# Kernel optimization log

Hardware: AMD Instinct MI355X
Metric: run time of the kernel (lower is better)

## Reference

```python
import jax, jax.numpy as jnp
import numpy as np
from jax import lax

K = 3          # kernel size
PAD = 1        # 'same' padding for k=3: (1,1,1,1)
STRIDE = 1
DIL = 1
OFFSET_SIZE = 2 * K * K  # deformable_groups=1


def setup_inputs() -> dict:
    key = jax.random.key(0)
    k1, k2, k3, k4 = jax.random.split(key, 4)
    B, H, W, C = 8, 64, 64, 256
    F = 256
    inputs = jax.random.normal(k1, (B, H, W, C), dtype=jnp.float32)
    # offset/mask branch conv: small weights so sampled offsets are modest
    om_kernel = jax.random.normal(k2, (K, K, C, OFFSET_SIZE * 3 // 2), dtype=jnp.float32) * 0.01
    om_bias = jnp.zeros((OFFSET_SIZE * 3 // 2,), dtype=jnp.float32)
    stdv = 1.0 / np.sqrt(K * K * C)
    kernel = jax.random.uniform(k3, (K * K * C, F), dtype=jnp.float32, minval=-stdv, maxval=stdv)
    bias = jax.random.normal(k4, (1, 1, 1, F), dtype=jnp.float32) * 0.01
    return {"inputs": inputs, "om_kernel": om_kernel, "om_bias": om_bias,
            "kernel": kernel, "bias": bias}


def _dcnv2(x, om_kernel, om_bias, kernel, bias):
    B, H, W, C = x.shape
    # offset/mask branch (same conv geometry as the deformable conv)
    om = lax.conv_general_dilated(
        x, om_kernel, window_strides=(STRIDE, STRIDE),
        padding=((PAD, PAD), (PAD, PAD)), rhs_dilation=(DIL, DIL),
        dimension_numbers=('NHWC', 'HWIO', 'NHWC')) + om_bias
    OH, OW = om.shape[1], om.shape[2]
    KK = K * K
    offset = om[..., :OFFSET_SIZE].reshape(B, OH, OW, KK, 2)  # (dy, dx) per kernel point
    mask = jax.nn.sigmoid(om[..., OFFSET_SIZE:]) * 2.0         # [B,OH,OW,KK]

    # base sampling grid per output pixel and kernel point
    kk = jnp.arange(KK)
    ky = (kk // K).astype(jnp.float32)
    kx = (kk % K).astype(jnp.float32)
    base_y = jnp.arange(OH, dtype=jnp.float32)[:, None] * STRIDE - PAD + ky[None, :] * DIL  # [OH,KK]
    base_x = jnp.arange(OW, dtype=jnp.float32)[:, None] * STRIDE - PAD + kx[None, :] * DIL  # [OW,KK]

    py = base_y[None, :, None, :] + offset[..., 0]  # [B,OH,OW,KK]
    px = base_x[None, None, :, :] + offset[..., 1]

    y0 = jnp.floor(py); x0 = jnp.floor(px)
    wy1 = py - y0; wy0 = 1.0 - wy1
    wx1 = px - x0; wx0 = 1.0 - wx1

    bi = jnp.arange(B)[:, None, None, None]

    def gather(yi, xi):
        # zero-padded bilinear corner fetch
        valid = (yi >= 0) & (yi <= H - 1) & (xi >= 0) & (xi <= W - 1)
        yc = jnp.clip(yi, 0, H - 1).astype(jnp.int32)
        xc = jnp.clip(xi, 0, W - 1).astype(jnp.int32)
        v = x[bi, yc, xc]  # [B,OH,OW,KK,C]
        return v * valid[..., None].astype(x.dtype)

    y1 = y0 + 1.0; x1 = x0 + 1.0
    cols = (gather(y0, x0) * (wy0 * wx0)[..., None]
            + gather(y0, x1) * (wy0 * wx1)[..., None]
            + gather(y1, x0) * (wy1 * wx0)[..., None]
            + gather(y1, x1) * (wy1 * wx1)[..., None])
    cols = cols * mask[..., None]  # modulation, [B,OH,OW,KK,C]

    out = cols.reshape(B, OH, OW, KK * C) @ kernel  # [B,OH,OW,F]
    return out + bias


def reference(inputs, om_kernel, om_bias, kernel, bias):
    return _dcnv2(inputs, om_kernel, om_bias, kernel, bias)
```

## Files before the change

kernel.cpp:

```cpp
#include <hip/hip_runtime.h>
#include <math.h>


#define BB 8
#define HH 64
#define WW 64
#define CIN 256
#define FF 256
#define KPTS 9
#define OCH 27
#define MT 64
#define NS2 36

typedef _Float16 half8  __attribute__((ext_vector_type(8)));
typedef _Float16 half4v __attribute__((ext_vector_type(4)));
typedef float    floatx4 __attribute__((ext_vector_type(4)));

__device__ __forceinline__ int aoff(int m, int g) {
    return m * 64 + ((g ^ (m & 7)) << 3);
}

__device__ __forceinline__ half8 splat8(_Float16 v) {
    half8 r = {v, v, v, v, v, v, v, v};
    return r;
}

#define XBLK 4096
__global__ __launch_bounds__(256) void convert_all(
    const float* __restrict__ x, const float* __restrict__ wmat,
    const float* __restrict__ omw,
    _Float16* __restrict__ xh, _Float16* __restrict__ wsB, _Float16* __restrict__ wsOM)
{
    const int bid = blockIdx.x;
    if (bid < XBLK) {
        if (xh == nullptr) return;
        const size_t i = ((size_t)bid * 256 + threadIdx.x) * 8;
        const floatx4 a = *(const floatx4*)(x + i);
        const floatx4 b = *(const floatx4*)(x + i + 4);
        half8 h;
        h[0] = (_Float16)a.x; h[1] = (_Float16)a.y; h[2] = (_Float16)a.z; h[3] = (_Float16)a.w;
        h[4] = (_Float16)b.x; h[5] = (_Float16)b.y; h[6] = (_Float16)b.z; h[7] = (_Float16)b.w;
        *(half8*)(xh + i) = h;
    } else if (bid < XBLK + 288) {
        const int kg = bid - XBLK;
        const int n  = threadIdx.x;
        half8 h;
        #pragma unroll
        for (int j = 0; j < 8; ++j)
            h[j] = (_Float16)wmat[(size_t)(kg * 8 + j) * FF + n];
        ((half8*)wsB)[(size_t)kg * FF + n] = h;
    } else {
        const int t = (bid - XBLK - 288) * 256 + threadIdx.x;
        const int k = t >> 5, n = t & 31;
        const float v = (n < OCH) ? omw[k * OCH + n] : 0.f;
        wsOM[((size_t)(k >> 3) * 32 + n) * 8 + (k & 7)] = (_Float16)v;
    }
}

template <bool F16X>
__global__ __launch_bounds__(512, 4) void dcn_mfma3(
    const float* __restrict__ x,
    const _Float16* __restrict__ xh,
    const float* __restrict__ omb,
    const _Float16* __restrict__ wsB,
    const _Float16* __restrict__ wsOM,
    const float* __restrict__ bias,
    float* __restrict__ out)
{
    __shared__ _Float16 Ah0[MT * 64];
    __shared__ _Float16 Ah1[MT * 64];
    __shared__ float    om_s[MT][28];
    __shared__ half4v   cwS[MT][KPTS];
    __shared__ int4     caS[MT][KPTS];

    const int tid  = threadIdx.x;
    const int w    = tid >> 6;
    const int lane = tid & 63;
    const int q    = lane >> 4;
    const int lr   = lane & 15;
    const int ms   = tid >> 3;
    const int qc   = tid & 7;

    const int p  = blockIdx.x;
    const int b  = p & 7;
    const int oh = p >> 3;
    const int pbase = (b * HH + oh) * WW;

    const half8* wsOM8 = (const half8*)wsOM;
    const half8* wsB8  = (const half8*)wsB;

    const int mt1 = w & 3;
    const int nt1 = w >> 2;
    floatx4 acc1 = {0.f, 0.f, 0.f, 0.f};

    auto load1 = [&](int sp) -> half8 {
        sp = sp < NS2 - 1 ? sp : NS2 - 1;
        const int kk = sp >> 2, cb = (sp & 3) << 6;
        const int ky = kk / 3, kx = kk - ky * 3;
        const int iy = oh - 1 + ky, ix = ms - 1 + kx;
        half8 v = {(_Float16)0, (_Float16)0, (_Float16)0, (_Float16)0,
                   (_Float16)0, (_Float16)0, (_Float16)0, (_Float16)0};
        if (iy >= 0 && iy < HH && ix >= 0 && ix < WW) {
            const int idx = ((b * HH + iy) * WW + ix) * CIN + cb + qc * 8;
            if constexpr (F16X) {
                v = *(const half8*)(xh + idx);
            } else {
                const floatx4 lo = *(const floatx4*)(x + idx);
                const floatx4 hi = *(const floatx4*)(x + idx + 4);
                v[0] = (_Float16)lo.x; v[1] = (_Float16)lo.y;
                v[2] = (_Float16)lo.z; v[3] = (_Float16)lo.w;
                v[4] = (_Float16)hi.x; v[5] = (_Float16)hi.y;
                v[6] = (_Float16)hi.z; v[7] = (_Float16)hi.w;
            }
        }
        return v;
    };
    auto loadB1 = [&](int sp, half8& b0, half8& b1) {
        sp = sp < NS2 - 1 ? sp : NS2 - 1;
        b0 = wsOM8[(sp * 8 + q) * 32 + nt1 * 16 + lr];
        b1 = wsOM8[(sp * 8 + 4 + q) * 32 + nt1 * 16 + lr];
    };

    half8 vp;
    half8 bo00, bo01, bo10, bo11;
    {
        const half8 v0 = load1(0);
        *(half8*)(Ah0 + aoff(ms, qc)) = v0;
        vp = load1(1);
        loadB1(0, bo00, bo01);
    }
    for (int s = 0; s < NS2; s += 2) {
        __syncthreads();
        *(half8*)(Ah1 + aoff(ms, qc)) = vp;
        vp = load1(s + 2);
        loadB1(s + 1, bo10, bo11);
        {
            const half8 a0 = *(const half8*)(Ah0 + aoff(mt1 * 16 + lr, q));
            const half8 a1 = *(const half8*)(Ah0 + aoff(mt1 * 16 + lr, 4 + q));
            acc1 = __builtin_amdgcn_mfma_f32_16x16x32_f16(a0, bo00, acc1, 0, 0, 0);
            acc1 = __builtin_amdgcn_mfma_f32_16x16x32_f16(a1, bo01, acc1, 0, 0, 0);
        }
        __syncthreads();
        *(half8*)(Ah0 + aoff(ms, qc)) = vp;
        vp = load1(s + 3);
        loadB1(s + 2, bo00, bo01);
        {
            const half8 a0 = *(const half8*)(Ah1 + aoff(mt1 * 16 + lr, q));
            const half8 a1 = *(const half8*)(Ah1 + aoff(mt1 * 16 + lr, 4 + q));
            acc1 = __builtin_amdgcn_mfma_f32_16x16x32_f16(a0, bo10, acc1, 0, 0, 0);
            acc1 = __builtin_amdgcn_mfma_f32_16x16x32_f16(a1, bo11, acc1, 0, 0, 0);
        }
    }
    {
        const int och = nt1 * 16 + lr;
        if (och < OCH) {
            const float ob = omb[och];
            #pragma unroll
            for (int reg = 0; reg < 4; ++reg) {
                const int m = mt1 * 16 + q * 4 + reg;
                om_s[m][och] = acc1[reg] + ob;
            }
        }
    }
    __syncthreads();

    for (int i = tid; i < MT * KPTS; i += 512) {
        const int m = i / KPTS, kk = i % KPTS;
        const int ky = kk / 3, kx = kk - ky * 3;
        const float dy = om_s[m][2 * kk];
        const float dx = om_s[m][2 * kk + 1];
        const float mask = 2.f / (1.f + __expf(-om_s[m][18 + kk]));
        const float py = (float)(oh - 1 + ky) + dy;
        const float px = (float)(m - 1 + kx) + dx;
        const float y0f = floorf(py), x0f = floorf(px);
        const float wy1 = py - y0f, wx1 = px - x0f;
        const float wy0 = 1.f - wy1, wx0 = 1.f - wx1;
        const int y0 = (int)y0f, x0 = (int)x0f;
        const int y1 = y0 + 1, x1 = x0 + 1;
        const bool vy0 = (y0 >= 0) && (y0 < HH);
        const bool vy1 = (y1 >= 0) && (y1 < HH);
        const bool vx0 = (x0 >= 0) && (x0 < WW);
        const bool vx1 = (x1 >= 0) && (x1 < WW);
        const int y0c = min(max(y0, 0), HH - 1), y1c = min(max(y1, 0), HH - 1);
        const int x0c = min(max(x0, 0), WW - 1), x1c = min(max(x1, 0), WW - 1);
        const int rb = b * HH;
        int4 ca;
        ca.x = ((rb + y0c) * WW + x0c) * CIN;
        ca.y = ((rb + y0c) * WW + x1c) * CIN;
        ca.z = ((rb + y1c) * WW + x0c) * CIN;
        ca.w = ((rb + y1c) * WW + x1c) * CIN;
        half4v cw;
        cw.x = (_Float16)((vy0 && vx0) ? mask * wy0 * wx0 : 0.f);
        cw.y = (_Float16)((vy0 && vx1) ? mask * wy0 * wx1 : 0.f);
        cw.z = (_Float16)((vy1 && vx0) ? mask * wy1 * wx0 : 0.f);
        cw.w = (_Float16)((vy1 && vx1) ? mask * wy1 * wx1 : 0.f);
        caS[m][kk] = ca;
        cwS[m][kk] = cw;
    }
    __syncthreads();

    floatx4 acc[4][2];
    #pragma unroll
    for (int mt = 0; mt < 4; ++mt)
        #pragma unroll
        for (int nt = 0; nt < 2; ++nt)
            acc[mt][nt] = (floatx4){0.f, 0.f, 0.f, 0.f};

    const int n0w = w * 32;

    half8   pc0, pc1, pc2, pc3;
    floatx4 fa0, fb0, fa1, fb1, fa2, fb2, fa3, fb3;
    half4v  pcw;

    auto pre2 = [&](int sp) {
        sp = sp < NS2 - 1 ? sp : NS2 - 1;
        const int kk = sp >> 2;
        const int co = ((sp & 3) << 6) + qc * 8;
        const int4 ca = caS[ms][kk];
        pcw = cwS[ms][kk];
        if constexpr (F16X) {
            pc0 = *(const half8*)(xh + ca.x + co);
            pc1 = *(const half8*)(xh + ca.y + co);
            pc2 = *(const half8*)(xh + ca.z + co);
            pc3 = *(const half8*)(xh + ca.w + co);
        } else {
            fa0 = *(const floatx4*)(x + ca.x + co); fb0 = *(const floatx4*)(x + ca.x + co + 4);
            fa1 = *(const floatx4*)(x + ca.y + co); fb1 = *(const floatx4*)(x + ca.y + co + 4);
            fa2 = *(const floatx4*)(x + ca.z + co); fb2 = *(const floatx4*)(x + ca.z + co + 4);
            fa3 = *(const floatx4*)(x + ca.w + co); fb3 = *(const floatx4*)(x + ca.w + co + 4);
        }
    };
    auto comb = [&]() -> half8 {
        if constexpr (F16X) {
            const half8 w0 = splat8(pcw.x), w1 = splat8(pcw.y);
            const half8 w2 = splat8(pcw.z), w3 = splat8(pcw.w);
            return pc0 * w0 + pc1 * w1 + pc2 * w2 + pc3 * w3;
        } else {
            const float w0 = (float)pcw.x, w1 = (float)pcw.y;
            const float w2 = (float)pcw.z, w3 = (float)pcw.w;
            const floatx4 lo = w0 * fa0 + w1 * fa1 + w2 * fa2 + w3 * fa3;
            const floatx4 hi = w0 * fb0 + w1 * fb1 + w2 * fb2 + w3 * fb3;
            half8 r;
            r[0] = (_Float16)lo.x; r[1] = (_Float16)lo.y;
            r[2] = (_Float16)lo.z; r[3] = (_Float16)lo.w;
            r[4] = (_Float16)hi.x; r[5] = (_Float16)hi.y;
            r[6] = (_Float16)hi.z; r[7] = (_Float16)hi.w;
            return r;
        }
    };

    half8 bPa[2][2], bPb[2][2];
    auto loadB2 = [&](int sp, half8 (&bP)[2][2]) {
        sp = sp < NS2 - 1 ? sp : NS2 - 1;
        #pragma unroll
        for (int kh = 0; kh < 2; ++kh)
            #pragma unroll
            for (int nt = 0; nt < 2; ++nt)
                bP[kh][nt] = wsB8[(size_t)(sp * 8 + kh * 4 + q) * FF + n0w + nt * 16 + lr];
    };

    {
        pre2(0);
        const half8 v0 = comb();
        *(half8*)(Ah0 + aoff(ms, qc)) = v0;
        pre2(1);
        loadB2(0, bPa);
    }
    for (int s = 0; s < NS2; s += 2) {
        __syncthreads();
        {
            const half8 v = comb();
            *(half8*)(Ah1 + aoff(ms, qc)) = v;
        }
        pre2(s + 2);
        loadB2(s + 1, bPb);
        #pragma unroll
        for (int kh = 0; kh < 2; ++kh) {
            half8 afr[4];
            #pragma unroll
            for (int mt = 0; mt < 4; ++mt)
                afr[mt] = *(const half8*)(Ah0 + aoff(mt * 16 + lr, kh * 4 + q));
            #pragma unroll
            for (int nt = 0; nt < 2; ++nt)
                #pragma unroll
                for (int mt = 0; mt < 4; ++mt)
                    acc[mt][nt] = __builtin_amdgcn_mfma_f32_16x16x32_f16(afr[mt], bPa[kh][nt], acc[mt][nt], 0, 0, 0);
        }
        __syncthreads();
        {
            const half8 v = comb();
            *(half8*)(Ah0 + aoff(ms, qc)) = v;
        }
        pre2(s + 3);
        loadB2(s + 2, bPa);
        #pragma unroll
        for (int kh = 0; kh < 2; ++kh) {
            half8 afr[4];
            #pragma unroll
            for (int mt = 0; mt < 4; ++mt)
                afr[mt] = *(const half8*)(Ah1 + aoff(mt * 16 + lr, kh * 4 + q));
            #pragma unroll
            for (int nt = 0; nt < 2; ++nt)
                #pragma unroll
                for (int mt = 0; mt < 4; ++mt)
                    acc[mt][nt] = __builtin_amdgcn_mfma_f32_16x16x32_f16(afr[mt], bPb[kh][nt], acc[mt][nt], 0, 0, 0);
        }
    }

    #pragma unroll
    for (int nt = 0; nt < 2; ++nt) {
        const int f = n0w + nt * 16 + lr;
        const float bv = bias[f];
        #pragma unroll
        for (int mt = 0; mt < 4; ++mt)
            #pragma unroll
            for (int reg = 0; reg < 4; ++reg) {
                const int m = mt * 16 + q * 4 + reg;
                out[(size_t)(pbase + m) * FF + f] = acc[mt][nt][reg] + bv;
            }
    }
}

#define MTILE 32
#define CHUNK 64
#define NCHUNK (CIN / CHUNK)

__global__ __launch_bounds__(256) void dcn_fused(
    const float* __restrict__ x, const float* __restrict__ omw,
    const float* __restrict__ omb, const float* __restrict__ wmat,
    const float* __restrict__ bias, float* __restrict__ out)
{
    __shared__ float A[CHUNK][MTILE + 1];
    __shared__ float om_s[MTILE][28];
    __shared__ float cw[MTILE][4];
    __shared__ int   ca[MTILE][4];

    const int tid = threadIdx.x;
    const int pbase = blockIdx.x * MTILE;
    const int ccid = tid & 63;
    const int mg2 = tid >> 6;
    const int och = tid & 31;
    const int mg1 = tid >> 5;
    float acc1[4] = {0.f, 0.f, 0.f, 0.f};

    for (int kk = 0; kk < KPTS; ++kk) {
        const int ky = kk / 3, kx = kk % 3;
        for (int ch = 0; ch < NCHUNK; ++ch) {
            const int cbase = ch * CHUNK;
            __syncthreads();
            #pragma unroll
            for (int i = 0; i < 8; ++i) {
                const int m = mg2 * 8 + i;
                const int pp = pbase + m;
                const int bb = pp >> 12, oh = (pp >> 6) & 63, ow = pp & 63;
                const int iy = oh - 1 + ky, ix = ow - 1 + kx;
                float v = 0.f;
                if (iy >= 0 && iy < HH && ix >= 0 && ix < WW)
                    v = x[((bb * HH + iy) * WW + ix) * CIN + cbase + ccid];
                A[ccid][m] = v;
            }
            __syncthreads();
            if (och < OCH) {
                for (int cc = 0; cc < CHUNK; ++cc) {
                    const float bv = omw[((kk * CIN) + cbase + cc) * OCH + och];
                    #pragma unroll
                    for (int i = 0; i < 4; ++i)
                        acc1[i] += A[cc][mg1 * 4 + i] * bv;
                }
            }
        }
    }
    __syncthreads();
    if (och < OCH) {
        const float ob = omb[och];
        #pragma unroll
        for (int i = 0; i < 4; ++i)
            om_s[mg1 * 4 + i][och] = acc1[i] + ob;
    }
    __syncthreads();

    const int f4 = (tid & 63) * 4;
    const int mgc = tid >> 6;
    float acc[8][4];
    #pragma unroll
    for (int j = 0; j < 8; ++j)
        #pragma unroll
        for (int i = 0; i < 4; ++i) acc[j][i] = 0.f;

    for (int kk = 0; kk < KPTS; ++kk) {
        if (tid < MTILE) {
            const int m = tid;
            const int pp = pbase + m;
            const int bb = pp >> 12, oh = (pp >> 6) & 63, ow = pp & 63;
            const int ky = kk / 3, kx = kk % 3;
            const float dy = om_s[m][2 * kk];
            const float dx = om_s[m][2 * kk + 1];
            const float mask = 2.f / (1.f + __expf(-om_s[m][18 + kk]));
            const float py = (float)(oh - 1 + ky) + dy;
            const float px = (float)(ow - 1 + kx) + dx;
            const float y0f = floorf(py), x0f = floorf(px);
            const float wy1 = py - y0f, wx1 = px - x0f;
            const float wy0 = 1.f - wy1, wx0 = 1.f - wx1;
            const int y0 = (int)y0f, x0 = (int)x0f;
            const int y1 = y0 + 1, x1 = x0 + 1;
            const bool vy0 = (y0 >= 0) && (y0 < HH);
            const bool vy1 = (y1 >= 0) && (y1 < HH);
            const bool vx0 = (x0 >= 0) && (x0 < WW);
            const bool vx1 = (x1 >= 0) && (x1 < WW);
            const int y0c = min(max(y0, 0), HH - 1), y1c = min(max(y1, 0), HH - 1);
            const int x0c = min(max(x0, 0), WW - 1), x1c = min(max(x1, 0), WW - 1);
            const int rb = bb * HH;
            ca[m][0] = ((rb + y0c) * WW + x0c) * CIN;
            ca[m][1] = ((rb + y0c) * WW + x1c) * CIN;
            ca[m][2] = ((rb + y1c) * WW + x0c) * CIN;
            ca[m][3] = ((rb + y1c) * WW + x1c) * CIN;
            cw[m][0] = (vy0 && vx0) ? mask * wy0 * wx0 : 0.f;
            cw[m][1] = (vy0 && vx1) ? mask * wy0 * wx1 : 0.f;
            cw[m][2] = (vy1 && vx0) ? mask * wy1 * wx0 : 0.f;
            cw[m][3] = (vy1 && vx1) ? mask * wy1 * wx1 : 0.f;
        }
        for (int ch = 0; ch < NCHUNK; ++ch) {
            const int cbase = ch * CHUNK;
            __syncthreads();
            #pragma unroll
            for (int i = 0; i < 8; ++i) {
                const int m = mg2 * 8 + i;
                const int cidx = cbase + ccid;
                const float v = cw[m][0] * x[ca[m][0] + cidx]
                              + cw[m][1] * x[ca[m][1] + cidx]
                              + cw[m][2] * x[ca[m][2] + cidx]
                              + cw[m][3] * x[ca[m][3] + cidx];
                A[ccid][m] = v;
            }
            __syncthreads();
            const float* brow = wmat + (size_t)(kk * CIN + cbase) * FF + f4;
            for (int cc = 0; cc < CHUNK; ++cc) {
                const float4 bv = *(const float4*)(brow + cc * FF);
                #pragma unroll
                for (int j = 0; j < 8; ++j) {
                    const float a = A[cc][mgc * 8 + j];
                    acc[j][0] += a * bv.x;
                    acc[j][1] += a * bv.y;
                    acc[j][2] += a * bv.z;
                    acc[j][3] += a * bv.w;
                }
            }
        }
    }

    const float4 bb4 = *(const float4*)(bias + f4);
    #pragma unroll
    for (int j = 0; j < 8; ++j) {
        const int m = mgc * 8 + j;
        const int pp = pbase + m;
        float4 o;
        o.x = acc[j][0] + bb4.x;
        o.y = acc[j][1] + bb4.y;
        o.z = acc[j][2] + bb4.z;
        o.w = acc[j][3] + bb4.w;
        *(float4*)(out + (size_t)pp * FF + f4) = o;
    }
}

extern "C" void kernel_launch(void* const* d_in, const int* in_sizes, int n_in,
                              void* d_out, int out_size, void* d_ws, size_t ws_size,
                              hipStream_t stream) {
    const float* x    = (const float*)d_in[0];
    const float* omw  = (const float*)d_in[1];
    const float* omb  = (const float*)d_in[2];
    const float* wmat = (const float*)d_in[3];
    const float* bias = (const float*)d_in[4];
    float* out = (float*)d_out;

    const size_t needB  = (size_t)2304 * FF * sizeof(_Float16);
    const size_t needOM = (size_t)288 * 32 * 8 * sizeof(_Float16);
    const size_t needX  = (size_t)BB * HH * WW * CIN * sizeof(_Float16);

    if (ws_size >= needB + needOM + needX) {
        _Float16* wsB  = (_Float16*)d_ws;
        _Float16* wsOM = (_Float16*)((char*)d_ws + needB);
        _Float16* xh   = (_Float16*)((char*)d_ws + needB + needOM);
        convert_all<<<XBLK + 288 + 288, 256, 0, stream>>>(x, wmat, omw, xh, wsB, wsOM);
        dcn_mfma3<true><<<BB * HH, 512, 0, stream>>>(x, xh, omb, wsB, wsOM, bias, out);
    } else if (ws_size >= needB + needOM) {
        _Float16* wsB  = (_Float16*)d_ws;
        _Float16* wsOM = (_Float16*)((char*)d_ws + needB);
        convert_all<<<XBLK + 288 + 288, 256, 0, stream>>>(x, wmat, omw, nullptr, wsB, wsOM);
        dcn_mfma3<false><<<BB * HH, 512, 0, stream>>>(x, nullptr, omb, wsB, wsOM, bias, out);
    } else {
        const int nblocks = (BB * HH * WW) / MTILE;
        dcn_fused<<<nblocks, 256, 0, stream>>>(x, omw, omb, wmat, bias, out);
    }
}
```

Baseline: 163.1 us.

## Retile MFMA warps to 2x4 M/N split and reorder K steps channel-major

Each of the 8 warps now covers 32 rows by 64 output channels instead of 64 rows by 32 channels. This halves the per-warp LDS A-fragment reads and doubles B-fragment register loads. The K-step order changes from kernel-point-major to channel-chunk-major via a divide-by-9 trick, so consecutive steps visit different sampling points. B fragments are now loaded just before use instead of prefetched one step ahead, which may expose global load latency.

```diff
diff --git a/kernel.cpp b/kernel.cpp
--- a/kernel.cpp
+++ b/kernel.cpp
@@ -58,7 +58,7 @@
 }
 
 template <bool F16X>
-__global__ __launch_bounds__(512, 4) void dcn_mfma3(
+__global__ __launch_bounds__(512, 4) void dcn_mfma4(
     const float* __restrict__ x,
     const _Float16* __restrict__ xh,
     const float* __restrict__ omb,
@@ -199,14 +199,16 @@
     }
     __syncthreads();
 
-    floatx4 acc[4][2];
+    floatx4 acc[2][4];
     #pragma unroll
-    for (int mt = 0; mt < 4; ++mt)
-        #pragma unroll
-        for (int nt = 0; nt < 2; ++nt)
-            acc[mt][nt] = (floatx4){0.f, 0.f, 0.f, 0.f};
-
-    const int n0w = w * 32;
+    for (int t = 0; t < 2; ++t)
+        #pragma unroll
+        for (int nt = 0; nt < 4; ++nt)
+            acc[t][nt] = (floatx4){0.f, 0.f, 0.f, 0.f};
+
+    const int mh  = w & 1;
+    const int nh  = w >> 1;
+    const int n0w = nh * 64;
 
     half8   pc0, pc1, pc2, pc3;
     floatx4 fa0, fb0, fa1, fb1, fa2, fb2, fa3, fb3;
@@ -214,8 +216,9 @@
 
     auto pre2 = [&](int sp) {
         sp = sp < NS2 - 1 ? sp : NS2 - 1;
-        const int kk = sp >> 2;
-        const int co = ((sp & 3) << 6) + qc * 8;
+        const int c  = (sp * 456) >> 12;
+        const int kk = sp - c * 9;
+        const int co = c * 64 + qc * 8;
         const int4 ca = caS[ms][kk];
         pcw = cwS[ms][kk];
         if constexpr (F16X) {
@@ -249,14 +252,16 @@
         }
     };
 
-    half8 bPa[2][2], bPb[2][2];
-    auto loadB2 = [&](int sp, half8 (&bP)[2][2]) {
-        sp = sp < NS2 - 1 ? sp : NS2 - 1;
+    half8 bP[2][4];
+    auto loadB2 = [&](int sp) {
+        const int c  = (sp * 456) >> 12;
+        const int kk = sp - c * 9;
+        const int r8 = kk * 32 + c * 8;
         #pragma unroll
         for (int kh = 0; kh < 2; ++kh)
             #pragma unroll
-            for (int nt = 0; nt < 2; ++nt)
-                bP[kh][nt] = wsB8[(size_t)(sp * 8 + kh * 4 + q) * FF + n0w + nt * 16 + lr];
+            for (int nt = 0; nt < 4; ++nt)
+                bP[kh][nt] = wsB8[(size_t)(r8 + kh * 4 + q) * FF + n0w + nt * 16 + lr];
     };
 
     {
@@ -264,7 +269,6 @@
         const half8 v0 = comb();
         *(half8*)(Ah0 + aoff(ms, qc)) = v0;
         pre2(1);
-        loadB2(0, bPa);
     }
     for (int s = 0; s < NS2; s += 2) {
         __syncthreads();
@@ -272,51 +276,51 @@
             const half8 v = comb();
             *(half8*)(Ah1 + aoff(ms, qc)) = v;
         }
+        loadB2(s);
         pre2(s + 2);
-        loadB2(s + 1, bPb);
         #pragma unroll
         for (int kh = 0; kh < 2; ++kh) {
-            half8 afr[4];
-            #pragma unroll
-            for (int mt = 0; mt < 4; ++mt)
-                afr[mt] = *(const half8*)(Ah0 + aoff(mt * 16 + lr, kh * 4 + q));
-            #pragma unroll
-            for (int nt = 0; nt < 2; ++nt)
+            half8 afr[2];
+            #pragma unroll
+            for (int t = 0; t < 2; ++t)
+                afr[t] = *(const half8*)(Ah0 + aoff((mh * 2 + t) * 16 + lr, kh * 4 + q));
+            #pragma unroll
+            for (int nt = 0; nt < 4; ++nt)
                 #pragma unroll
-                for (int mt = 0; mt < 4; ++mt)
-                    acc[mt][nt] = __builtin_amdgcn_mfma_f32_16x16x32_f16(afr[mt], bPa[kh][nt], acc[mt][nt], 0, 0, 0);
+                for (int t = 0; t < 2; ++t)
+                    acc[t][nt] = __builtin_amdgcn_mfma_f32_16x16x32_f16(afr[t], bP[kh][nt], acc[t][nt], 0, 0, 0);
         }
         __syncthreads();
         {
             const half8 v = comb();
             *(half8*)(Ah0 + aoff(ms, qc)) = v;
         }
+        loadB2(s + 1);
         pre2(s + 3);
-        loadB2(s + 2, bPa);
         #pragma unroll
         for (int kh = 0; kh < 2; ++kh) {
-            half8 afr[4];
-            #pragma unroll
-            for (int mt = 0; mt < 4; ++mt)
-                afr[mt] = *(const half8*)(Ah1 + aoff(mt * 16 + lr, kh * 4 + q));
-            #pragma unroll
-            for (int nt = 0; nt < 2; ++nt)
+            half8 afr[2];
+            #pragma unroll
+            for (int t = 0; t < 2; ++t)
+                afr[t] = *(const half8*)(Ah1 + aoff((mh * 2 + t) * 16 + lr, kh * 4 + q));
+            #pragma unroll
+            for (int nt = 0; nt < 4; ++nt)
                 #pragma unroll
-                for (int mt = 0; mt < 4; ++mt)
-                    acc[mt][nt] = __builtin_amdgcn_mfma_f32_16x16x32_f16(afr[mt], bPb[kh][nt], acc[mt][nt], 0, 0, 0);
+                for (int t = 0; t < 2; ++t)
+                    acc[t][nt] = __builtin_amdgcn_mfma_f32_16x16x32_f16(afr[t], bP[kh][nt], acc[t][nt], 0, 0, 0);
         }
     }
 
     #pragma unroll
-    for (int nt = 0; nt < 2; ++nt) {
+    for (int nt = 0; nt < 4; ++nt) {
         const int f = n0w + nt * 16 + lr;
         const float bv = bias[f];
         #pragma unroll
-        for (int mt = 0; mt < 4; ++mt)
+        for (int t = 0; t < 2; ++t)
             #pragma unroll
             for (int reg = 0; reg < 4; ++reg) {
-                const int m = mt * 16 + q * 4 + reg;
-                out[(size_t)(pbase + m) * FF + f] = acc[mt][nt][reg] + bv;
+                const int m = (mh * 2 + t) * 16 + q * 4 + reg;
+                out[(size_t)(pbase + m) * FF + f] = acc[t][nt][reg] + bv;
             }
     }
 }
@@ -481,12 +485,12 @@
         _Float16* wsOM = (_Float16*)((char*)d_ws + needB);
         _Float16* xh   = (_Float16*)((char*)d_ws + needB + needOM);
         convert_all<<<XBLK + 288 + 288, 256, 0, stream>>>(x, wmat, omw, xh, wsB, wsOM);
-        dcn_mfma3<true><<<BB * HH, 512, 0, stream>>>(x, xh, omb, wsB, wsOM, bias, out);
+        dcn_mfma4<true><<<BB * HH, 512, 0, stream>>>(x, xh, omb, wsB, wsOM, bias, out);
     } else if (ws_size >= needB + needOM) {
         _Float16* wsB  = (_Float16*)d_ws;
         _Float16* wsOM = (_Float16*)((char*)d_ws + needB);
         convert_all<<<XBLK + 288 + 288, 256, 0, stream>>>(x, wmat, omw, nullptr, wsB, wsOM);
-        dcn_mfma3<false><<<BB * HH, 512, 0, stream>>>(x, nullptr, omb, wsB, wsOM, bias, out);
+        dcn_mfma4<false><<<BB * HH, 512, 0, stream>>>(x, nullptr, omb, wsB, wsOM, bias, out);
     } else {
         const int nblocks = (BB * HH * WW) / MTILE;
         dcn_fused<<<nblocks, 256, 0, stream>>>(x, omw, omb, wmat, bias, out);
```

Measured after the change: 166.9 us. +2.4%, slower.
